# Kernel tuning notes

Measured on AMD Instinct MI355X. Metric: run time of the kernel, lower is better.

The kernel has to match this reference:

```python
import jax, jax.numpy as jnp
import numpy as np


def setup_inputs() -> dict:
    key = jax.random.key(0)
    kq, kk, kv, km = jax.random.split(key, 4)
    B, H, S, D = 4, 16, 2048, 64
    query = jax.random.normal(kq, (B, H, S, D), dtype=jnp.float32)
    k = jax.random.normal(kk, (B, H, S, D), dtype=jnp.float32)
    value = jax.random.normal(kv, (B, H, S, D), dtype=jnp.float32)
    mask = jax.random.randint(km, (B, S, S), 0, 2, dtype=jnp.int32)
    return {"query": query, "key": k, "value": value, "mask": mask}


def reference(query, key, value, mask):
    # query/key/value: [B, H, S, D]; mask: [B, S, S] (0 = masked out)
    d = query.shape[-1]
    scale = 1.0 / jnp.sqrt(jnp.asarray(d, dtype=query.dtype))
    scores = jnp.einsum('bhqd,bhkd->bhqk', query, key) * scale
    m = (mask[:, None, :, :] == 0)  # broadcast over heads, matches mask.unsqueeze(1).eq(0)
    min_value = jnp.finfo(scores.dtype).min
    scores = jnp.where(m, min_value, scores)
    attn = jax.nn.softmax(scores, axis=-1)
    attn = jnp.where(m, jnp.asarray(0.0, attn.dtype), attn)
    out = jnp.einsum('bhqk,bhkd->bhqd', attn, value)
    return (out, attn)
```

## Files before the change

### kernel.cpp

```cpp
#include <hip/hip_runtime.h>


typedef __attribute__((ext_vector_type(8))) short bf16x8;
typedef __attribute__((ext_vector_type(4))) float f32x4;
typedef __attribute__((ext_vector_type(4))) int i32x4;
typedef __attribute__((ext_vector_type(2))) unsigned int u32x2;

#define MFMA16(A, B, C) __builtin_amdgcn_mfma_f32_16x16x32_bf16((A), (B), (C), 0, 0, 0)

constexpr int Bsz = 4, Hsz = 16, Ssz = 2048, Dsz = 64;
constexpr int QBLK = 64;
constexpr int KBLK = 64;
constexpr int NTHR = 512;
constexpr float SCALE = 0.125f;

static __device__ __forceinline__ short f2bf(float f) {
  unsigned u = __float_as_uint(f);
  u = (u + 0x7fffu + ((u >> 16) & 1u)) >> 16;
  return (short)u;
}

__global__ __launch_bounds__(NTHR, 4)
void attn_fused(const float* __restrict__ Qg, const float* __restrict__ Kg,
                const float* __restrict__ Vg, const int* __restrict__ Mg,
                float* __restrict__ Og, float* __restrict__ Ag)
{
  __shared__ __align__(16) char smem[3 * 64 * 72 * 2];
  short (*sK)[72]  = (short(*)[72])(smem);
  short (*sVt)[72] = (short(*)[72])(smem + 9216);
  short (*sP)[72]  = (short(*)[72])(smem + 18432);
  float (*sO)[68]  = (float(*)[68])(smem);
  __shared__ float sL[2][QBLK];

  const int qt   = blockIdx.x;
  const int bh   = blockIdx.y;
  const int q0   = qt * QBLK;
  const int tid  = threadIdx.x;
  const int lane = tid & 63;
  const int wid  = tid >> 6;
  const int wq   = wid >> 1;
  const int wk   = wid & 1;
  const int lr   = lane & 15;
  const int lg   = lane >> 4;

  const size_t bhSD = (size_t)bh * (Ssz * Dsz);
  const float* Qb = Qg + bhSD;
  const float* Kb = Kg + bhSD;
  const float* Vb = Vg + bhSD;
  const int*   Mb = Mg + (size_t)(bh >> 4) * ((size_t)Ssz * Ssz);
  float*       Ob = Og + bhSD;
  float*       Ab = Ag + (size_t)bh * ((size_t)Ssz * Ssz);

  const int qrow = q0 + wq * 16 + lr;

  bf16x8 qf[2];
  {
    const float* qp = Qb + (size_t)qrow * Dsz + lg * 8;
#pragma unroll
    for (int h = 0; h < 2; ++h) {
      f32x4 a = *(const f32x4*)(qp + h * 32);
      f32x4 b = *(const f32x4*)(qp + h * 32 + 4);
      bf16x8 t;
#pragma unroll
      for (int j = 0; j < 4; ++j) { t[j] = f2bf(a[j] * SCALE); t[4 + j] = f2bf(b[j] * SCALE); }
      qf[h] = t;
    }
  }

  const int krow = tid >> 3;
  const int kd0  = (tid & 7) * 8;
  const int vkv  = tid & 63;
  const int vd0  = (tid >> 6) * 8;
  const int kb0  = wk * 32 + lg * 4;

  float lacc = 0.f;

  for (int kt = 0; kt < Ssz; kt += KBLK) {
    __syncthreads();
    i32x4 m0 = *(const i32x4*)(Mb + (size_t)qrow * Ssz + kt + kb0);
    i32x4 m1 = *(const i32x4*)(Mb + (size_t)qrow * Ssz + kt + kb0 + 16);
    {
      const float* kp = Kb + (size_t)(kt + krow) * Dsz + kd0;
      f32x4 a = *(const f32x4*)kp;
      f32x4 b = *(const f32x4*)(kp + 4);
      bf16x8 t;
#pragma unroll
      for (int j = 0; j < 4; ++j) { t[j] = f2bf(a[j]); t[4 + j] = f2bf(b[j]); }
      *(bf16x8*)(&sK[krow][kd0]) = t;
    }
    __syncthreads();
#pragma unroll
    for (int cb = 0; cb < 2; ++cb) {
      const short* kr = &sK[wk * 32 + cb * 16 + lr][0];
      bf16x8 a0 = *(const bf16x8*)(kr + lg * 8);
      bf16x8 a1 = *(const bf16x8*)(kr + 32 + lg * 8);
      f32x4 c = {0.f, 0.f, 0.f, 0.f};
      c = MFMA16(a0, qf[0], c);
      c = MFMA16(a1, qf[1], c);
      i32x4 mv = cb ? m1 : m0;
#pragma unroll
      for (int r = 0; r < 4; ++r) lacc += mv[r] ? __expf(c[r]) : 0.f;
    }
  }

  lacc += __shfl_xor(lacc, 16, 64);
  lacc += __shfl_xor(lacc, 32, 64);
  if (lane < 16) sL[wk][wq * 16 + lane] = lacc;
  __syncthreads();
  const float lsum = sL[0][wq * 16 + lr] + sL[1][wq * 16 + lr];
  const float invl = (lsum > 0.f) ? 1.f / lsum : 0.f;

  f32x4 oacc[4] = {{0,0,0,0},{0,0,0,0},{0,0,0,0},{0,0,0,0}};

  for (int kt = 0; kt < Ssz; kt += KBLK) {
    __syncthreads();
    i32x4 m0 = *(const i32x4*)(Mb + (size_t)qrow * Ssz + kt + kb0);
    i32x4 m1 = *(const i32x4*)(Mb + (size_t)qrow * Ssz + kt + kb0 + 16);
    {
      const float* kp = Kb + (size_t)(kt + krow) * Dsz + kd0;
      f32x4 a = *(const f32x4*)kp;
      f32x4 b = *(const f32x4*)(kp + 4);
      bf16x8 t;
#pragma unroll
      for (int j = 0; j < 4; ++j) { t[j] = f2bf(a[j]); t[4 + j] = f2bf(b[j]); }
      *(bf16x8*)(&sK[krow][kd0]) = t;

      const float* vp = Vb + (size_t)(kt + vkv) * Dsz + vd0;
      f32x4 va = *(const f32x4*)vp;
      f32x4 vb = *(const f32x4*)(vp + 4);
#pragma unroll
      for (int j = 0; j < 4; ++j) {
        sVt[vd0 + j][vkv]     = f2bf(va[j]);
        sVt[vd0 + 4 + j][vkv] = f2bf(vb[j]);
      }
    }
    __syncthreads();
#pragma unroll
    for (int cb = 0; cb < 2; ++cb) {
      const short* kr = &sK[wk * 32 + cb * 16 + lr][0];
      bf16x8 a0 = *(const bf16x8*)(kr + lg * 8);
      bf16x8 a1 = *(const bf16x8*)(kr + 32 + lg * 8);
      f32x4 c = {0.f, 0.f, 0.f, 0.f};
      c = MFMA16(a0, qf[0], c);
      c = MFMA16(a1, qf[1], c);
      i32x4 mv = cb ? m1 : m0;
      f32x4 p;
#pragma unroll
      for (int r = 0; r < 4; ++r) p[r] = mv[r] ? __expf(c[r]) * invl : 0.f;
      __builtin_nontemporal_store(p, (f32x4*)(Ab + (size_t)qrow * Ssz + kt + kb0 + cb * 16));
      unsigned plo = (unsigned short)f2bf(p[0]) | ((unsigned)(unsigned short)f2bf(p[1]) << 16);
      unsigned phi = (unsigned short)f2bf(p[2]) | ((unsigned)(unsigned short)f2bf(p[3]) << 16);
      u32x2 w = {plo, phi};
      *(u32x2*)(&sP[wq * 16 + lr][wk * 32 + cb * 16 + lg * 4]) = w;
    }
    bf16x8 pa = *(const bf16x8*)(&sP[wq * 16 + lr][wk * 32 + lg * 8]);
#pragma unroll
    for (int nb = 0; nb < 4; ++nb) {
      bf16x8 vb = *(const bf16x8*)(&sVt[nb * 16 + lr][wk * 32 + lg * 8]);
      oacc[nb] = MFMA16(pa, vb, oacc[nb]);
    }
  }

  __syncthreads();
  if (wk == 0) {
#pragma unroll
    for (int nb = 0; nb < 4; ++nb)
#pragma unroll
      for (int r = 0; r < 4; ++r)
        sO[wq * 16 + lg * 4 + r][nb * 16 + lr] = oacc[nb][r];
  }
  __syncthreads();
  if (wk == 1) {
#pragma unroll
    for (int nb = 0; nb < 4; ++nb)
#pragma unroll
      for (int r = 0; r < 4; ++r) {
        float v = sO[wq * 16 + lg * 4 + r][nb * 16 + lr] + oacc[nb][r];
        __builtin_nontemporal_store(v, Ob + (size_t)(q0 + wq * 16 + lg * 4 + r) * Dsz + nb * 16 + lr);
      }
  }
}

extern "C" void kernel_launch(void* const* d_in, const int* in_sizes, int n_in,
                              void* d_out, int out_size, void* d_ws, size_t ws_size,
                              hipStream_t stream) {
  const float* Q = (const float*)d_in[0];
  const float* K = (const float*)d_in[1];
  const float* V = (const float*)d_in[2];
  const int*   M = (const int*)d_in[3];
  float* Out  = (float*)d_out;
  float* Attn = Out + (size_t)Bsz * Hsz * Ssz * Dsz;
  dim3 grid(Ssz / QBLK, Bsz * Hsz);
  attn_fused<<<grid, NTHR, 0, stream>>>(Q, K, V, M, Out, Attn);
}
```

Measured before the change: 521.1 us.

## Double-buffer K/V tiles in LDS with register prefetch and lighter barriers

```diff
diff --git a/kernel.cpp b/kernel.cpp
--- a/kernel.cpp
+++ b/kernel.cpp
@@ -12,12 +12,21 @@
 constexpr int QBLK = 64;
 constexpr int KBLK = 64;
 constexpr int NTHR = 512;
+constexpr int NT   = Ssz / KBLK;
 constexpr float SCALE = 0.125f;
 
 static __device__ __forceinline__ short f2bf(float f) {
   unsigned u = __float_as_uint(f);
   u = (u + 0x7fffu + ((u >> 16) & 1u)) >> 16;
   return (short)u;
+}
+
+static __device__ __forceinline__ void wg_barrier() {
+  __builtin_amdgcn_sched_barrier(0);
+  asm volatile("s_waitcnt lgkmcnt(0)" ::: "memory");
+  __builtin_amdgcn_sched_barrier(0);
+  __builtin_amdgcn_s_barrier();
+  __builtin_amdgcn_sched_barrier(0);
 }
 
 __global__ __launch_bounds__(NTHR, 4)
@@ -25,11 +34,11 @@
                 const float* __restrict__ Vg, const int* __restrict__ Mg,
                 float* __restrict__ Og, float* __restrict__ Ag)
 {
-  __shared__ __align__(16) char smem[3 * 64 * 72 * 2];
-  short (*sK)[72]  = (short(*)[72])(smem);
-  short (*sVt)[72] = (short(*)[72])(smem + 9216);
-  short (*sP)[72]  = (short(*)[72])(smem + 18432);
-  float (*sO)[68]  = (float(*)[68])(smem);
+  __shared__ __align__(16) char smem[5 * 64 * 72 * 2];
+  auto sK  = (short(*)[KBLK][72])(smem);
+  auto sVt = (short(*)[Dsz][72])(smem + 2 * 9216);
+  auto sP  = (short(*)[72])(smem + 4 * 9216);
+  auto sO  = (float(*)[68])(smem);
   __shared__ float sL[2][QBLK];
 
   const int qt   = blockIdx.x;
@@ -52,6 +61,8 @@
   float*       Ab = Ag + (size_t)bh * ((size_t)Ssz * Ssz);
 
   const int qrow = q0 + wq * 16 + lr;
+  const int* Mrow = Mb + (size_t)qrow * Ssz;
+  float*     Arow = Ab + (size_t)qrow * Ssz;
 
   bf16x8 qf[2];
   {
@@ -73,25 +84,34 @@
   const int vd0  = (tid >> 6) * 8;
   const int kb0  = wk * 32 + lg * 4;
 
+  {
+    const float* kp = Kb + (size_t)krow * Dsz + kd0;
+    f32x4 a = *(const f32x4*)kp;
+    f32x4 b = *(const f32x4*)(kp + 4);
+    bf16x8 t;
+#pragma unroll
+    for (int j = 0; j < 4; ++j) { t[j] = f2bf(a[j]); t[4 + j] = f2bf(b[j]); }
+    *(bf16x8*)(&sK[0][krow][kd0]) = t;
+  }
+  i32x4 m0n = *(const i32x4*)(Mrow + kb0);
+  i32x4 m1n = *(const i32x4*)(Mrow + kb0 + 16);
+  wg_barrier();
+
   float lacc = 0.f;
-
-  for (int kt = 0; kt < Ssz; kt += KBLK) {
-    __syncthreads();
-    i32x4 m0 = *(const i32x4*)(Mb + (size_t)qrow * Ssz + kt + kb0);
-    i32x4 m1 = *(const i32x4*)(Mb + (size_t)qrow * Ssz + kt + kb0 + 16);
-    {
-      const float* kp = Kb + (size_t)(kt + krow) * Dsz + kd0;
-      f32x4 a = *(const f32x4*)kp;
-      f32x4 b = *(const f32x4*)(kp + 4);
-      bf16x8 t;
-#pragma unroll
-      for (int j = 0; j < 4; ++j) { t[j] = f2bf(a[j]); t[4 + j] = f2bf(b[j]); }
-      *(bf16x8*)(&sK[krow][kd0]) = t;
-    }
-    __syncthreads();
+  for (int t = 0; t < NT; ++t) {
+    const int cur = t & 1;
+    const i32x4 m0 = m0n, m1 = m1n;
+    f32x4 ka = {0.f, 0.f, 0.f, 0.f}, kb2 = {0.f, 0.f, 0.f, 0.f};
+    if (t + 1 < NT) {
+      const float* kp = Kb + (size_t)((t + 1) * KBLK + krow) * Dsz + kd0;
+      ka  = *(const f32x4*)kp;
+      kb2 = *(const f32x4*)(kp + 4);
+      m0n = *(const i32x4*)(Mrow + (t + 1) * KBLK + kb0);
+      m1n = *(const i32x4*)(Mrow + (t + 1) * KBLK + kb0 + 16);
+    }
 #pragma unroll
     for (int cb = 0; cb < 2; ++cb) {
-      const short* kr = &sK[wk * 32 + cb * 16 + lr][0];
+      const short* kr = &sK[cur][wk * 32 + cb * 16 + lr][0];
       bf16x8 a0 = *(const bf16x8*)(kr + lg * 8);
       bf16x8 a1 = *(const bf16x8*)(kr + 32 + lg * 8);
       f32x4 c = {0.f, 0.f, 0.f, 0.f};
@@ -101,43 +121,64 @@
 #pragma unroll
       for (int r = 0; r < 4; ++r) lacc += mv[r] ? __expf(c[r]) : 0.f;
     }
+    if (t + 1 < NT) {
+      bf16x8 tt;
+#pragma unroll
+      for (int j = 0; j < 4; ++j) { tt[j] = f2bf(ka[j]); tt[4 + j] = f2bf(kb2[j]); }
+      *(bf16x8*)(&sK[cur ^ 1][krow][kd0]) = tt;
+    }
+    wg_barrier();
   }
 
   lacc += __shfl_xor(lacc, 16, 64);
   lacc += __shfl_xor(lacc, 32, 64);
   if (lane < 16) sL[wk][wq * 16 + lane] = lacc;
-  __syncthreads();
+  wg_barrier();
   const float lsum = sL[0][wq * 16 + lr] + sL[1][wq * 16 + lr];
   const float invl = (lsum > 0.f) ? 1.f / lsum : 0.f;
 
   f32x4 oacc[4] = {{0,0,0,0},{0,0,0,0},{0,0,0,0},{0,0,0,0}};
 
-  for (int kt = 0; kt < Ssz; kt += KBLK) {
-    __syncthreads();
-    i32x4 m0 = *(const i32x4*)(Mb + (size_t)qrow * Ssz + kt + kb0);
-    i32x4 m1 = *(const i32x4*)(Mb + (size_t)qrow * Ssz + kt + kb0 + 16);
-    {
-      const float* kp = Kb + (size_t)(kt + krow) * Dsz + kd0;
-      f32x4 a = *(const f32x4*)kp;
-      f32x4 b = *(const f32x4*)(kp + 4);
-      bf16x8 t;
-#pragma unroll
-      for (int j = 0; j < 4; ++j) { t[j] = f2bf(a[j]); t[4 + j] = f2bf(b[j]); }
-      *(bf16x8*)(&sK[krow][kd0]) = t;
-
-      const float* vp = Vb + (size_t)(kt + vkv) * Dsz + vd0;
-      f32x4 va = *(const f32x4*)vp;
-      f32x4 vb = *(const f32x4*)(vp + 4);
-#pragma unroll
-      for (int j = 0; j < 4; ++j) {
-        sVt[vd0 + j][vkv]     = f2bf(va[j]);
-        sVt[vd0 + 4 + j][vkv] = f2bf(vb[j]);
-      }
-    }
-    __syncthreads();
+  {
+    const float* kp = Kb + (size_t)krow * Dsz + kd0;
+    f32x4 a = *(const f32x4*)kp;
+    f32x4 b = *(const f32x4*)(kp + 4);
+    bf16x8 t;
+#pragma unroll
+    for (int j = 0; j < 4; ++j) { t[j] = f2bf(a[j]); t[4 + j] = f2bf(b[j]); }
+    *(bf16x8*)(&sK[0][krow][kd0]) = t;
+
+    const float* vp = Vb + (size_t)vkv * Dsz + vd0;
+    f32x4 va = *(const f32x4*)vp;
+    f32x4 vb = *(const f32x4*)(vp + 4);
+#pragma unroll
+    for (int j = 0; j < 4; ++j) {
+      sVt[0][vd0 + j][vkv]     = f2bf(va[j]);
+      sVt[0][vd0 + 4 + j][vkv] = f2bf(vb[j]);
+    }
+  }
+  m0n = *(const i32x4*)(Mrow + kb0);
+  m1n = *(const i32x4*)(Mrow + kb0 + 16);
+  wg_barrier();
+
+  for (int t = 0; t < NT; ++t) {
+    const int cur = t & 1;
+    const i32x4 m0 = m0n, m1 = m1n;
+    f32x4 ka = {0.f,0.f,0.f,0.f}, kb2 = {0.f,0.f,0.f,0.f};
+    f32x4 va = {0.f,0.f,0.f,0.f}, vb2 = {0.f,0.f,0.f,0.f};
+    if (t + 1 < NT) {
+      const float* kp = Kb + (size_t)((t + 1) * KBLK + krow) * Dsz + kd0;
+      ka  = *(const f32x4*)kp;
+      kb2 = *(const f32x4*)(kp + 4);
+      const float* vp = Vb + (size_t)((t + 1) * KBLK + vkv) * Dsz + vd0;
+      va  = *(const f32x4*)vp;
+      vb2 = *(const f32x4*)(vp + 4);
+      m0n = *(const i32x4*)(Mrow + (t + 1) * KBLK + kb0);
+      m1n = *(const i32x4*)(Mrow + (t + 1) * KBLK + kb0 + 16);
+    }
 #pragma unroll
     for (int cb = 0; cb < 2; ++cb) {
-      const short* kr = &sK[wk * 32 + cb * 16 + lr][0];
+      const short* kr = &sK[cur][wk * 32 + cb * 16 + lr][0];
       bf16x8 a0 = *(const bf16x8*)(kr + lg * 8);
       bf16x8 a1 = *(const bf16x8*)(kr + 32 + lg * 8);
       f32x4 c = {0.f, 0.f, 0.f, 0.f};
@@ -147,7 +188,7 @@
       f32x4 p;
 #pragma unroll
       for (int r = 0; r < 4; ++r) p[r] = mv[r] ? __expf(c[r]) * invl : 0.f;
-      __builtin_nontemporal_store(p, (f32x4*)(Ab + (size_t)qrow * Ssz + kt + kb0 + cb * 16));
+      __builtin_nontemporal_store(p, (f32x4*)(Arow + t * KBLK + kb0 + cb * 16));
       unsigned plo = (unsigned short)f2bf(p[0]) | ((unsigned)(unsigned short)f2bf(p[1]) << 16);
       unsigned phi = (unsigned short)f2bf(p[2]) | ((unsigned)(unsigned short)f2bf(p[3]) << 16);
       u32x2 w = {plo, phi};
@@ -156,12 +197,23 @@
     bf16x8 pa = *(const bf16x8*)(&sP[wq * 16 + lr][wk * 32 + lg * 8]);
 #pragma unroll
     for (int nb = 0; nb < 4; ++nb) {
-      bf16x8 vb = *(const bf16x8*)(&sVt[nb * 16 + lr][wk * 32 + lg * 8]);
+      bf16x8 vb = *(const bf16x8*)(&sVt[cur][nb * 16 + lr][wk * 32 + lg * 8]);
       oacc[nb] = MFMA16(pa, vb, oacc[nb]);
     }
-  }
-
-  __syncthreads();
+    if (t + 1 < NT) {
+      bf16x8 tt;
+#pragma unroll
+      for (int j = 0; j < 4; ++j) { tt[j] = f2bf(ka[j]); tt[4 + j] = f2bf(kb2[j]); }
+      *(bf16x8*)(&sK[cur ^ 1][krow][kd0]) = tt;
+#pragma unroll
+      for (int j = 0; j < 4; ++j) {
+        sVt[cur ^ 1][vd0 + j][vkv]     = f2bf(va[j]);
+        sVt[cur ^ 1][vd0 + 4 + j][vkv] = f2bf(vb2[j]);
+      }
+    }
+    wg_barrier();
+  }
+
   if (wk == 0) {
 #pragma unroll
     for (int nb = 0; nb < 4; ++nb)
@@ -169,7 +221,7 @@
       for (int r = 0; r < 4; ++r)
         sO[wq * 16 + lg * 4 + r][nb * 16 + lr] = oacc[nb][r];
   }
-  __syncthreads();
+  wg_barrier();
   if (wk == 1) {
 #pragma unroll
     for (int nb = 0; nb < 4; ++nb)
```

New measurement: 503.0 us. 1.04x faster.
